# Kernel tuning notes

Hardware: AMD Instinct MI355X
Metric: run time of the kernel (lower is better)

## Reference

```python
import jax, jax.numpy as jnp
import numpy as np

B, N, M = 2, 256, 256  # batch items, bboxes per item, feature dim (output_channel)
BLOCKS = 2             # graph_conv_block_num


def _conv2d(x, w, b):
    # x: [C,H,W], w: [O,I,kh,kw] -> [O,H,W], SAME padding, stride 1
    y = jax.lax.conv_general_dilated(x[None], w, (1, 1), 'SAME',
                                     dimension_numbers=('NCHW', 'OIHW', 'NCHW'))
    return y[0] + b[:, None, None]


def setup_inputs() -> dict:
    key = jax.random.key(0)
    ks = jax.random.split(key, 8)
    s = 0.02  # small init to keep activations tame through conv stack
    return {
        'edge_feats': jax.random.normal(ks[0], (B, N, N, 7), jnp.float32),
        'node_feats': jax.random.normal(ks[1], (B, N, M), jnp.float32),
        'adapter_w': jax.random.normal(ks[2], (M, 7, 1, 1), jnp.float32) * s,
        'adapter_b': jnp.zeros((M,), jnp.float32),
        'conv0_w': jax.random.normal(ks[3], (M, 3 * M, 3, 3), jnp.float32) * s,
        'conv0_b': jnp.zeros((M,), jnp.float32),
        'conv1_w': jax.random.normal(ks[4], (M, M, 3, 3), jnp.float32) * s,
        'conv1_b': jnp.zeros((M,), jnp.float32),
        'last_w': jax.random.normal(ks[5], (M, M, 3, 3), jnp.float32) * s,
        'last_b': jnp.zeros((M,), jnp.float32),
        'att_w': jax.random.normal(ks[6], (1, M, 1, 1), jnp.float32) * s,
        'att_b': jnp.zeros((1,), jnp.float32),
    }


def reference(edge_feats, node_feats, adapter_w, adapter_b, conv0_w, conv0_b,
              conv1_w, conv1_b, last_w, last_b, att_w, att_b):
    def one(e, n):
        # e: [N,N,7], n: [N,M]
        edge = _conv2d(jnp.transpose(e, (2, 0, 1)), adapter_w, adapter_b)  # [M,N,N]
        node = n
        for _ in range(BLOCKS):  # conv weights shared across blocks, as in torch
            nT = node.T  # [M,N]
            # channel layout at (i,j): [node_i | edge_ij | node_j]
            feat = jnp.concatenate([
                jnp.broadcast_to(nT[:, :, None], (M, N, N)),
                edge,
                jnp.broadcast_to(nT[:, None, :], (M, N, N)),
            ], axis=0)  # [3M,N,N]
            feat = jax.nn.relu(_conv2d(feat, conv0_w, conv0_b))
            feat = jax.nn.relu(_conv2d(feat, conv1_w, conv1_b))
            # edge attention: 1x1 conv -> leaky_relu -> softmax over j -> weighted sum
            att = jax.nn.leaky_relu(_conv2d(feat, att_w, att_b))   # [1,N,N]
            coeff = jax.nn.softmax(att, axis=-1)                   # softmax over last dim
            node = jnp.sum(coeff * feat, axis=-1).T                # [N,M]
            edge = jax.nn.relu(_conv2d(feat, last_w, last_b))      # [M,N,N]
        return node, jnp.transpose(edge, (1, 2, 0))  # [N,M], [N,N,M]
    return jax.vmap(one)(edge_feats, node_feats)
```

## Files before the change

kernel.cpp:

```cpp
#include <hip/hip_runtime.h>
#include <hip/hip_bf16.h>

typedef __hip_bfloat16 bf16;
typedef __attribute__((ext_vector_type(8))) short s16x8;
typedef __attribute__((ext_vector_type(4))) float f32x4;

__device__ __forceinline__ float b2f(bf16 x) { return __bfloat162float(x); }
__device__ __forceinline__ bf16 f2b(float x) { return __float2bfloat16(x); }

__device__ __forceinline__ void gld16(const void* g, void* l) {
  __builtin_amdgcn_global_load_lds((const __attribute__((address_space(1))) unsigned int*)g,
                                   (__attribute__((address_space(3))) unsigned int*)l,
                                   16, 0, 0);
}

#define BARRIER() do { asm volatile("" ::: "memory"); \
                       __builtin_amdgcn_s_barrier();  \
                       asm volatile("" ::: "memory"); } while (0)

__global__ __launch_bounds__(256) void fill_sentinel(float* out, int n) {
  int idx = blockIdx.x * 256 + threadIdx.x;
  if (idx < n) out[idx] = 100.0f;
}

__global__ __launch_bounds__(64) void zero_zb(bf16* zb) {
  zb[threadIdx.x * 2] = f2b(0.f);
  zb[threadIdx.x * 2 + 1] = f2b(0.f);
}

__global__ __launch_bounds__(256) void pack_w(const float* __restrict__ c0w,
                                              const float* __restrict__ c1w,
                                              const float* __restrict__ lw,
                                              bf16* wp0, bf16* wp1, bf16* wp2, bf16* wnp) {
  const int SEG = 9 * 256 * 256;
  int idx = blockIdx.x * 256 + threadIdx.x;
  if (idx < 3 * SEG) {
    int which = idx / SEG, r = idx % SEG;
    int s = r >> 16, o = (r >> 8) & 255, c = r & 255;
    int ky = s / 3, kx = s - 3 * ky;
    if (which == 0)      wp0[r] = f2b(c0w[(((size_t)o * 768 + 256 + c) * 3 + ky) * 3 + kx]);
    else if (which == 1) wp1[r] = f2b(c1w[(((size_t)o * 256 + c) * 3 + ky) * 3 + kx]);
    else                 wp2[r] = f2b(lw [(((size_t)o * 256 + c) * 3 + ky) * 3 + kx]);
  } else {
    int r = idx - 3 * SEG;
    int m = r & 255, c = (r >> 8) & 255, tt = r >> 16;
    int ot = tt % 3, t2 = (tt / 3) % 3, p = tt / 9;
    int ky, kx, cin;
    if (p == 0) { kx = t2; ky = ot; cin = c; }
    else        { ky = t2; kx = ot; cin = 512 + c; }
    wnp[r] = f2b(c0w[(((size_t)m * 768 + cin) * 3 + ky) * 3 + kx]);
  }
}

__global__ __launch_bounds__(256) void adapter_k(const float* __restrict__ e,
                                                 const float* __restrict__ aw,
                                                 const float* __restrict__ ab,
                                                 bf16* __restrict__ E) {
  int i = blockIdx.x;
  int m = threadIdx.x;
  __shared__ float se[256 * 7];
  const size_t rb = (size_t)i * (256 * 7);
  for (int idx = m; idx < 256 * 7; idx += 256) se[idx] = e[rb + idx];
  __syncthreads();
  float w[7];
#pragma unroll
  for (int c = 0; c < 7; ++c) w[c] = aw[m * 7 + c];
  float bias = ab[m];
  bf16* ob = E + (size_t)i * 65536 + m;
  for (int j = 0; j < 256; ++j) {
    const float* ej = se + j * 7;
    float a = bias;
#pragma unroll
    for (int c = 0; c < 7; ++c) a += w[c] * ej[c];
    ob[(size_t)j * 256] = f2b(a);
  }
}

template <typename T>
__global__ __launch_bounds__(256) void node_terms(const T* __restrict__ nd,
                                                  const bf16* __restrict__ wnp,
                                                  float* __restrict__ TT) {
  int bid = blockIdx.x;
  int chunk = bid & 63;
  int t = (bid >> 6) % 3;
  int p = bid / 192;
  int tid = threadIdx.x;
  __shared__ float snd[6][256];
  int pos0 = chunk * 4;
  for (int idx = tid; idx < 6 * 256; idx += 256) {
    int r = idx >> 8, c = idx & 255;
    int gp = pos0 - 1 + r;
    snd[r][c] = (gp >= 0 && gp < 256) ? (float)nd[(size_t)gp * 256 + c] : 0.f;
  }
  __syncthreads();
  float acc[4] = {0.f, 0.f, 0.f, 0.f};
  const bf16* wb = wnp + (size_t)((p * 3 + t) * 3) * 65536 + tid;
  for (int c = 0; c < 256; ++c) {
    float w0 = b2f(wb[(size_t)c * 256]);
    float w1 = b2f(wb[(size_t)(65536 + c * 256)]);
    float w2 = b2f(wb[(size_t)(2 * 65536 + c * 256)]);
#pragma unroll
    for (int ii = 0; ii < 4; ++ii)
      acc[ii] += w0 * snd[ii][c] + w1 * snd[ii + 1][c] + w2 * snd[ii + 2][c];
  }
  float* o = TT + (((size_t)(p * 3 + t) * 256 + pos0) * 256) + tid;
#pragma unroll
  for (int ii = 0; ii < 4; ++ii) o[(size_t)ii * 256] = acc[ii];
}

template <int EPI, int F32OUT>
__global__ __launch_bounds__(512, 1)
void conv3x3_k(const bf16* __restrict__ inb, const bf16* __restrict__ wpack,
               const float* __restrict__ bias, void* __restrict__ outv,
               const float* __restrict__ TT, const bf16* __restrict__ zbuf) {
  __shared__ __align__(16) char lds[131072];
  const int bid = blockIdx.x;
  const int i = ((bid & 7) << 5) + (bid >> 3);
  const int tid = threadIdx.x;
  const int lane = tid & 63, wid = tid >> 6;
  const int wr = wid >> 2, wc = wid & 3;
  const int lo = lane & 15, hi = lane >> 4;
  const int Gs = tid & 7;

  f32x4 acc00[4][2], acc01[4][2], acc10[4][2], acc11[4][2];
  const f32x4 z = {0.f, 0.f, 0.f, 0.f};
#pragma unroll
  for (int mf = 0; mf < 4; ++mf)
#pragma unroll
    for (int nf = 0; nf < 2; ++nf) { acc00[mf][nf] = z; acc01[mf][nf] = z;
                                     acc10[mf][nf] = z; acc11[mf][nf] = z; }
  s16x8 af[4][2], bfr[2][2];

  const int s_lo = (i == 0) ? 3 : 0;
  const int s_hi = (i == 255) ? 5 : 8;
  const int nt = (s_hi - s_lo + 1) * 4;

  auto STAGE_IN = [&](int t, int r) {
    const int s = s_lo + (t >> 2);
    const int ky = s / 3, kx = s - 3 * ky;
    const int cb = (t & 3) * 64;
    const int x = r * 64 + (tid >> 3);
    const int j = x + kx - 1;
    const int sw = (Gs ^ (x & 7)) << 3;
    const bf16* src = (j >= 0 && j <= 255)
        ? inb + (size_t)(i + ky - 1) * 65536 + ((size_t)j << 8) + cb + sw
        : zbuf + sw;
    gld16(src, lds + (t & 1) * 65536 + ((r * 64 + wid * 8) << 7));
  };
  auto STAGE_W = [&](int t, int r) {
    const int s = s_lo + (t >> 2);
    const int cb = (t & 3) * 64;
    const int o = r * 64 + (tid >> 3);
    gld16(wpack + ((size_t)(s * 256 + o) << 8) + cb + ((Gs ^ (o & 7)) << 3),
          lds + (t & 1) * 65536 + 32768 + ((r * 64 + wid * 8) << 7));
  };
  auto LD_AF = [&](int buf, int mh) {
#pragma unroll
    for (int mf = 0; mf < 4; ++mf)
#pragma unroll
      for (int kk = 0; kk < 2; ++kk) {
        const int x = mh * 128 + wr * 64 + mf * 16 + lo;
        af[mf][kk] = *(const s16x8*)(lds + buf * 65536 + x * 128 +
                                     (((kk * 4 + hi) ^ (lo & 7)) << 4));
      }
  };
  auto LD_BF = [&](int buf, int nh) {
#pragma unroll
    for (int nf = 0; nf < 2; ++nf)
#pragma unroll
      for (int kk = 0; kk < 2; ++kk) {
        const int o = wc * 64 + nh * 32 + nf * 16 + lo;
        bfr[nf][kk] = *(const s16x8*)(lds + buf * 65536 + 32768 + o * 128 +
                                      (((kk * 4 + hi) ^ (lo & 7)) << 4));
      }
  };

#define MMA_Q(ACC)                                                            \
  __builtin_amdgcn_s_setprio(1);                                              \
  _Pragma("unroll") for (int mf = 0; mf < 4; ++mf)                            \
  _Pragma("unroll") for (int nf = 0; nf < 2; ++nf)                            \
  _Pragma("unroll") for (int kk = 0; kk < 2; ++kk)                            \
    ACC[mf][nf] = __builtin_amdgcn_mfma_f32_16x16x32_bf16(                    \
        af[mf][kk], bfr[nf][kk], ACC[mf][nf], 0, 0, 0);                       \
  __builtin_amdgcn_s_setprio(0);

#pragma unroll
  for (int r = 0; r < 4; ++r) { STAGE_IN(0, r); STAGE_W(0, r); }
  asm volatile("s_waitcnt vmcnt(0)" ::: "memory");
  BARRIER();

  for (int kt = 0; kt < nt; ++kt) {
    const int buf = kt & 1;
    const bool pf = (kt + 1 < nt);
    LD_AF(buf, 0); LD_BF(buf, 0);
    if (pf) { STAGE_W(kt + 1, 0); STAGE_W(kt + 1, 1); }
    BARRIER();
    MMA_Q(acc00);
    LD_BF(buf, 1);
    if (pf) { STAGE_W(kt + 1, 2); STAGE_W(kt + 1, 3); }
    if (pf) asm volatile("s_waitcnt vmcnt(4)" ::: "memory");
    else    asm volatile("s_waitcnt vmcnt(0)" ::: "memory");
    BARRIER();
    MMA_Q(acc01);
    LD_AF(buf, 1); LD_BF(buf, 0);
    if (pf) { STAGE_IN(kt + 1, 0); STAGE_IN(kt + 1, 1); }
    BARRIER();
    MMA_Q(acc10);
    LD_BF(buf, 1);
    if (pf) { STAGE_IN(kt + 1, 2); STAGE_IN(kt + 1, 3); }
    if (pf) asm volatile("s_waitcnt vmcnt(2)" ::: "memory");
    else    asm volatile("s_waitcnt vmcnt(0)" ::: "memory");
    BARRIER();
    MMA_Q(acc11);
  }
#undef MMA_Q

  bf16* orow = (bf16*)outv + (size_t)i * 65536;
  float* orowf = (float*)outv + (size_t)i * 65536;
#define EPI_Q(ACC, MH, NH)                                                    \
  _Pragma("unroll") for (int mf = 0; mf < 4; ++mf) {                          \
    _Pragma("unroll") for (int nf = 0; nf < 2; ++nf) {                        \
      const int o = wc * 64 + NH * 32 + nf * 16 + lo;                         \
      const float bs = bias[o];                                               \
      float ni0 = 0.f, ni1 = 0.f, ni2 = 0.f;                                  \
      if (EPI) { const float* TI = TT + (size_t)i * 256 + o;                  \
        ni0 = TI[0]; ni1 = TI[65536]; ni2 = TI[2 * 65536]; }                  \
      _Pragma("unroll") for (int rr = 0; rr < 4; ++rr) {                      \
        const int j = MH * 128 + wr * 64 + mf * 16 + hi * 4 + rr;             \
        float v = ACC[mf][nf][rr] + bs;                                       \
        if (EPI) {                                                            \
          v += ni1 + (j > 0 ? ni0 : 0.f) + (j < 255 ? ni2 : 0.f);             \
          const float* TJ = TT + (size_t)3 * 65536 + (size_t)j * 256 + o;     \
          float nj0 = TJ[0], nj1 = TJ[65536], nj2 = TJ[2 * 65536];            \
          v += nj1 + (i > 0 ? nj0 : 0.f) + (i < 255 ? nj2 : 0.f); }           \
        v = fmaxf(v, 0.f);                                                    \
        if (F32OUT) orowf[(size_t)j * 256 + o] = v;                           \
        else        orow[(size_t)j * 256 + o] = f2b(v);                       \
      } } }
  EPI_Q(acc00, 0, 0); EPI_Q(acc01, 0, 1); EPI_Q(acc10, 1, 0); EPI_Q(acc11, 1, 1);
#undef EPI_Q
}

template <int F32OUT>
__global__ __launch_bounds__(256) void att_wsum(const bf16* __restrict__ feat,
                                                const float* __restrict__ aw,
                                                const float* __restrict__ ab,
                                                bf16* __restrict__ ndb,
                                                float* __restrict__ ndf) {
  int i = blockIdx.x;
  int tid = threadIdx.x, lane = tid & 63, w = tid >> 6;
  __shared__ float s_aw[256];
  __shared__ float s_att[256];
  __shared__ float s_red[8];
  s_aw[tid] = aw[tid];
  __syncthreads();
  float a0 = s_aw[lane * 4], a1 = s_aw[lane * 4 + 1];
  float a2 = s_aw[lane * 4 + 2], a3 = s_aw[lane * 4 + 3];
  const bf16* fb = feat + (size_t)i * 65536;
  float abv = ab[0];
  for (int jj = 0; jj < 64; ++jj) {
    int j = w * 64 + jj;
    const bf16* f = fb + (size_t)j * 256 + lane * 4;
    float v = a0 * b2f(f[0]) + a1 * b2f(f[1]) + a2 * b2f(f[2]) + a3 * b2f(f[3]);
#pragma unroll
    for (int mk = 32; mk; mk >>= 1) v += __shfl_xor(v, mk);
    if (lane == 0) { float a = v + abv; s_att[j] = a > 0.f ? a : 0.01f * a; }
  }
  __syncthreads();
  float x = s_att[tid];
  float mx = x;
#pragma unroll
  for (int mk = 32; mk; mk >>= 1) mx = fmaxf(mx, __shfl_xor(mx, mk));
  if (lane == 0) s_red[w] = mx;
  __syncthreads();
  mx = fmaxf(fmaxf(s_red[0], s_red[1]), fmaxf(s_red[2], s_red[3]));
  float e = expf(x - mx);
  float sm = e;
#pragma unroll
  for (int mk = 32; mk; mk >>= 1) sm += __shfl_xor(sm, mk);
  if (lane == 0) s_red[4 + w] = sm;
  __syncthreads();
  sm = s_red[4] + s_red[5] + s_red[6] + s_red[7];
  __syncthreads();
  s_att[tid] = e / sm;
  __syncthreads();
  float acc = 0.f;
  for (int j = 0; j < 256; ++j) acc += s_att[j] * b2f(fb[(size_t)j * 256 + tid]);
  if (F32OUT) ndf[(size_t)i * 256 + tid] = acc;
  else        ndb[(size_t)i * 256 + tid] = f2b(acc);
}

extern "C" void kernel_launch(void* const* d_in, const int* in_sizes, int n_in,
                              void* d_out, int out_size, void* d_ws, size_t ws_size,
                              hipStream_t stream) {
  const float* edge_feats = (const float*)d_in[0];
  const float* node_feats = (const float*)d_in[1];
  const float* adapter_w  = (const float*)d_in[2];
  const float* adapter_b  = (const float*)d_in[3];
  const float* conv0_w    = (const float*)d_in[4];
  const float* conv0_b    = (const float*)d_in[5];
  const float* conv1_w    = (const float*)d_in[6];
  const float* conv1_b    = (const float*)d_in[7];
  const float* last_w     = (const float*)d_in[8];
  const float* last_b     = (const float*)d_in[9];
  const float* att_w      = (const float*)d_in[10];
  const float* att_b      = (const float*)d_in[11];
  float* out = (float*)d_out;

  char* ws = (char*)d_ws;
  size_t off = 0;
  bf16* Q   = (bf16*)(ws + off); off += (size_t)256 * 256 * 256 * 2;
  bf16* WP0 = (bf16*)(ws + off); off += (size_t)9 * 65536 * 2;
  bf16* WP1 = (bf16*)(ws + off); off += (size_t)9 * 65536 * 2;
  bf16* WP2 = (bf16*)(ws + off); off += (size_t)9 * 65536 * 2;
  bf16* WNP = (bf16*)(ws + off); off += (size_t)18 * 65536 * 2;
  float* TT = (float*)(ws + off); off += (size_t)2 * 3 * 65536 * 4;
  bf16* ND  = (bf16*)(ws + off); off += (size_t)65536 * 2;
  bf16* ZB  = (bf16*)(ws + off); off += 256;
  if (ws_size < off) {
    fill_sentinel<<<(out_size + 255) / 256, 256, 0, stream>>>(out, out_size);
    return;
  }

  zero_zb<<<1, 64, 0, stream>>>(ZB);
  pack_w<<<11520, 256, 0, stream>>>(conv0_w, conv1_w, last_w, WP0, WP1, WP2, WNP);

  for (int b = 0; b < 2; ++b) {
    bf16* P = (bf16*)(out + 131072 + (size_t)b * 16777216);
    float* edge_out = out + 131072 + (size_t)b * 16777216;
    float* node_out = out + (size_t)b * 65536;
    const float* eb = edge_feats + (size_t)b * 458752;
    const float* nb = node_feats + (size_t)b * 65536;

    adapter_k<<<256, 256, 0, stream>>>(eb, adapter_w, adapter_b, P);
    node_terms<float><<<384, 256, 0, stream>>>(nb, WNP, TT);
    conv3x3_k<1, 0><<<256, 512, 0, stream>>>(P, WP0, conv0_b, Q, TT, ZB);
    conv3x3_k<0, 0><<<256, 512, 0, stream>>>(Q, WP1, conv1_b, P, nullptr, ZB);
    att_wsum<0><<<256, 256, 0, stream>>>(P, att_w, att_b, ND, nullptr);
    conv3x3_k<0, 0><<<256, 512, 0, stream>>>(P, WP2, last_b, Q, nullptr, ZB);
    node_terms<bf16><<<384, 256, 0, stream>>>(ND, WNP, TT);
    conv3x3_k<1, 0><<<256, 512, 0, stream>>>(Q, WP0, conv0_b, P, TT, ZB);
    conv3x3_k<0, 0><<<256, 512, 0, stream>>>(P, WP1, conv1_b, Q, nullptr, ZB);
    att_wsum<1><<<256, 256, 0, stream>>>(Q, att_w, att_b, nullptr, node_out);
    conv3x3_k<0, 1><<<256, 512, 0, stream>>>(Q, WP2, last_b, edge_out, nullptr, ZB);
  }
}
```

Before: 1.248 ms.

## Keep both B-fragment halves in registers and issue prefetches earlier in conv GEMM

Loads both halves of the weight (B) fragments once per k-step into two separate register sets, so each half is reused across both M halves instead of being reloaded from LDS. It also reorders the global-to-LDS prefetches: all next-tile weight loads are issued at the start of the k-step and all input loads after the first MMA quarter. The vmcnt waits are relaxed so the second half of the input tile may still be in flight during the first MMA quarters. This cuts LDS read traffic and allows more load/compute overlap, at the cost of extra VGPRs for the second B-fragment set, which could lower occupancy.

```diff
diff --git a/kernel.cpp b/kernel.cpp
--- a/kernel.cpp
+++ b/kernel.cpp
@@ -129,7 +129,7 @@
 #pragma unroll
     for (int nf = 0; nf < 2; ++nf) { acc00[mf][nf] = z; acc01[mf][nf] = z;
                                      acc10[mf][nf] = z; acc11[mf][nf] = z; }
-  s16x8 af[4][2], bfr[2][2];
+  s16x8 af[4][2], bfr0[2][2], bfr1[2][2];
 
   const int s_lo = (i == 0) ? 3 : 0;
   const int s_hi = (i == 255) ? 5 : 8;
@@ -164,54 +164,54 @@
                                      (((kk * 4 + hi) ^ (lo & 7)) << 4));
       }
   };
-  auto LD_BF = [&](int buf, int nh) {
+  auto LD_BF = [&](int buf, int nh, s16x8 (&dst)[2][2]) {
 #pragma unroll
     for (int nf = 0; nf < 2; ++nf)
 #pragma unroll
       for (int kk = 0; kk < 2; ++kk) {
         const int o = wc * 64 + nh * 32 + nf * 16 + lo;
-        bfr[nf][kk] = *(const s16x8*)(lds + buf * 65536 + 32768 + o * 128 +
+        dst[nf][kk] = *(const s16x8*)(lds + buf * 65536 + 32768 + o * 128 +
                                       (((kk * 4 + hi) ^ (lo & 7)) << 4));
       }
   };
 
-#define MMA_Q(ACC)                                                            \
+#define MMA_Q(ACC, BFR)                                                       \
   __builtin_amdgcn_s_setprio(1);                                              \
   _Pragma("unroll") for (int mf = 0; mf < 4; ++mf)                            \
   _Pragma("unroll") for (int nf = 0; nf < 2; ++nf)                            \
   _Pragma("unroll") for (int kk = 0; kk < 2; ++kk)                            \
     ACC[mf][nf] = __builtin_amdgcn_mfma_f32_16x16x32_bf16(                    \
-        af[mf][kk], bfr[nf][kk], ACC[mf][nf], 0, 0, 0);                       \
+        af[mf][kk], BFR[nf][kk], ACC[mf][nf], 0, 0, 0);                       \
   __builtin_amdgcn_s_setprio(0);
 
 #pragma unroll
-  for (int r = 0; r < 4; ++r) { STAGE_IN(0, r); STAGE_W(0, r); }
-  asm volatile("s_waitcnt vmcnt(0)" ::: "memory");
+  for (int r = 0; r < 4; ++r) STAGE_W(0, r);
+#pragma unroll
+  for (int r = 0; r < 4; ++r) STAGE_IN(0, r);
+  asm volatile("s_waitcnt vmcnt(2)" ::: "memory");
   BARRIER();
 
   for (int kt = 0; kt < nt; ++kt) {
     const int buf = kt & 1;
     const bool pf = (kt + 1 < nt);
-    LD_AF(buf, 0); LD_BF(buf, 0);
-    if (pf) { STAGE_W(kt + 1, 0); STAGE_W(kt + 1, 1); }
+    LD_AF(buf, 0); LD_BF(buf, 0, bfr0);
+    if (pf) { STAGE_W(kt + 1, 0); STAGE_W(kt + 1, 1);
+              STAGE_W(kt + 1, 2); STAGE_W(kt + 1, 3); }
     BARRIER();
-    MMA_Q(acc00);
-    LD_BF(buf, 1);
-    if (pf) { STAGE_W(kt + 1, 2); STAGE_W(kt + 1, 3); }
-    if (pf) asm volatile("s_waitcnt vmcnt(4)" ::: "memory");
+    MMA_Q(acc00, bfr0);
+    LD_BF(buf, 1, bfr1);
+    if (pf) { STAGE_IN(kt + 1, 0); STAGE_IN(kt + 1, 1);
+              STAGE_IN(kt + 1, 2); STAGE_IN(kt + 1, 3); }
+    if (pf) asm volatile("s_waitcnt vmcnt(8)" ::: "memory");
     else    asm volatile("s_waitcnt vmcnt(0)" ::: "memory");
     BARRIER();
-    MMA_Q(acc01);
-    LD_AF(buf, 1); LD_BF(buf, 0);
-    if (pf) { STAGE_IN(kt + 1, 0); STAGE_IN(kt + 1, 1); }
+    MMA_Q(acc01, bfr1);
+    LD_AF(buf, 1);
     BARRIER();
-    MMA_Q(acc10);
-    LD_BF(buf, 1);
-    if (pf) { STAGE_IN(kt + 1, 2); STAGE_IN(kt + 1, 3); }
+    MMA_Q(acc10, bfr0);
     if (pf) asm volatile("s_waitcnt vmcnt(2)" ::: "memory");
-    else    asm volatile("s_waitcnt vmcnt(0)" ::: "memory");
     BARRIER();
-    MMA_Q(acc11);
+    MMA_Q(acc11, bfr1);
   }
 #undef MMA_Q
 
```

Measured after the change: 1.194 ms (median of 2 runs). 4.3% less time.
